# Optimization experiments

Measured on AMD Instinct MI355X. Metric: run time of the kernel, lower is better.

Reference implementation:

```python
import jax, jax.numpy as jnp
import numpy as np

T, N, E = 4, 20000, 640000
D_IN, D_OUT = 256, 128
RRELU_SLOPE = (1.0 / 8.0 + 1.0 / 3.0) / 2.0  # RReLU eval-mode slope


def setup_inputs() -> dict:
    key = jax.random.key(0)
    ks = jax.random.split(key, 16)

    def glorot(k, shape):
        lim = np.sqrt(6.0 / (shape[0] + shape[1]))
        return jax.random.uniform(k, shape, jnp.float32, -lim, lim)

    node_embs = jax.random.normal(ks[0], (T, N, D_IN), jnp.float32)
    edge_index = jax.random.randint(ks[1], (T, 2, E), 0, N, jnp.int32)
    edge_weight = jax.random.uniform(ks[2], (T, E), jnp.float32)
    mask = jnp.zeros((T, N), jnp.float32)
    return {
        "node_embs": node_embs,
        "edge_index": edge_index,
        "edge_weight": edge_weight,
        "mask": mask,
        "p": glorot(ks[3], (D_IN, 1)),
        "Wz": glorot(ks[4], (D_IN, D_IN)),
        "Uz": glorot(ks[5], (D_IN, D_IN)),
        "bz": jnp.zeros((D_IN, D_OUT), jnp.float32),
        "Wr": glorot(ks[6], (D_IN, D_IN)),
        "Ur": glorot(ks[7], (D_IN, D_IN)),
        "br": jnp.zeros((D_IN, D_OUT), jnp.float32),
        "Wh": glorot(ks[8], (D_IN, D_IN)),
        "Uh": glorot(ks[9], (D_IN, D_IN)),
        "bh": jnp.zeros((D_IN, D_OUT), jnp.float32),
        "W0": glorot(ks[10], (D_IN, D_OUT)),
    }


def reference(node_embs, edge_index, edge_weight, mask, p, Wz, Uz, bz, Wr, Ur, br, Wh, Uh, bh, W0):
    n = node_embs.shape[1]
    k = W0.shape[1]

    def step(W, inputs):
        x, ei, w, m = inputs  # x: [N, D_IN]
        # --- TopK summary (EvolveGCN-H) ---
        scores = (x @ p)[:, 0] / jnp.linalg.norm(p) + m  # [N]
        vals, idx = jax.lax.top_k(scores, k)
        xt = (x[idx] * jnp.tanh(vals)[:, None]).T  # [D_IN, k]
        # --- matrix GRU cell: hidden state is the GCN weight W ---
        z = jax.nn.sigmoid(Wz @ xt + Uz @ W + bz)
        r = jax.nn.sigmoid(Wr @ xt + Ur @ W + br)
        h = jnp.tanh(Wh @ xt + Uh @ (r * W) + bh)
        Wn = (1.0 - z) * W + z * h  # [D_IN, D_OUT]
        # --- sparse GCN conv: adj @ (x @ Wn) ---
        y = x @ Wn  # [N, D_OUT]
        dst, src = ei[0], ei[1]
        agg = jax.ops.segment_sum(w[:, None] * y[src], dst, num_segments=n)
        out = jnp.where(agg >= 0, agg, RRELU_SLOPE * agg)
        return Wn, out

    _, out_seq = jax.lax.scan(step, W0, (node_embs, edge_index, edge_weight, mask))
    return out_seq  # [T, N, D_OUT]
```

## Files before the change

kernel.cpp:

```cpp
#include <hip/hip_runtime.h>

typedef unsigned short u16;
typedef unsigned int u32;
typedef unsigned long long u64;

#define T_ 4
#define N_ 20000
#define E_ 640000
#define DIN 256
#define DOUT 128
#define NT (T_*N_)
#define TE (T_*E_)
#define SLOPE 0.22916666666666666f

#define NB 125
#define BNODES 160
#define CAP 5632
#define NBTOT (T_*NB)

#define SGRAN 11
#define NSB 10
#define NBIN (32*NSB*5)
#define NBIN_PAD 2048
#define BOSTRIDE 40

typedef __attribute__((ext_vector_type(8))) short short8;
typedef __attribute__((ext_vector_type(4))) float f32x4;

__device__ __forceinline__ float blo(u32 u) { return __uint_as_float(u << 16); }
__device__ __forceinline__ float bhi(u32 u) { return __uint_as_float(u & 0xFFFF0000u); }
__device__ __forceinline__ u16 f2bf(float f) {
    u32 u = __float_as_uint(f);
    return (u16)((u + 0x7FFFu + ((u >> 16) & 1u)) >> 16);
}
__device__ __forceinline__ u32 fkey(float f) {
    u32 u = __float_as_uint(f);
    return (u & 0x80000000u) ? ~u : (u | 0x80000000u);
}
__device__ __forceinline__ float fkeyinv(u32 k) {
    u32 u = (k & 0x80000000u) ? (k ^ 0x80000000u) : ~k;
    return __uint_as_float(u);
}

__global__ void k_transpose(const float* Wz, const float* Uz, const float* Wr, const float* Ur,
                            const float* Wh, const float* Uh, u32* Tp) {
    int bid = blockIdx.x;
    int m = bid >> 7, b = bid & 127;
    int idx = b * 256 + threadIdx.x;
    int d2 = idx & 127, i = idx >> 7;
    const float* src;
    switch (m) {
        case 0: src = Wz; break;
        case 1: src = Uz; break;
        case 2: src = Wr; break;
        case 3: src = Ur; break;
        case 4: src = Wh; break;
        default: src = Uh; break;
    }
    float lo = src[i * 256 + 2 * d2];
    float hi = src[i * 256 + 2 * d2 + 1];
    Tp[m * 32768 + d2 * 256 + i] = (u32)f2bf(lo) | ((u32)f2bf(hi) << 16);
}

__global__ __launch_bounds__(256) void k_scores(const float* x, const float* p, const float* mask,
                                                float* scores, u16* xb16) {
    __shared__ float pl[256];
    __shared__ float s_invn;
    int tid = threadIdx.x;
    pl[tid] = p[tid];
    __syncthreads();
    if (tid < 64) {
        float v = pl[tid] * pl[tid] + pl[tid + 64] * pl[tid + 64] +
                  pl[tid + 128] * pl[tid + 128] + pl[tid + 192] * pl[tid + 192];
        for (int o = 32; o > 0; o >>= 1) v += __shfl_xor(v, o);
        if (tid == 0) s_invn = 1.0f / sqrtf(v);
    }
    __syncthreads();
    int wid = tid >> 6, lane = tid & 63;
    for (int it = 0; it < 4; ++it) {
        int node = blockIdx.x * 16 + wid * 4 + it;
        const float* row = x + (size_t)node * DIN + lane * 4;
        float4 u = *(const float4*)row;
        float d = u.x * pl[lane * 4 + 0] + u.y * pl[lane * 4 + 1] +
                  u.z * pl[lane * 4 + 2] + u.w * pl[lane * 4 + 3];
        u32 p0 = (u32)f2bf(u.x) | ((u32)f2bf(u.y) << 16);
        u32 p1 = (u32)f2bf(u.z) | ((u32)f2bf(u.w) << 16);
        *(uint2*)(xb16 + (size_t)node * DIN + lane * 4) = make_uint2(p0, p1);
        for (int o = 32; o > 0; o >>= 1) d += __shfl_xor(d, o);
        if (lane == 0) scores[node] = d * s_invn + mask[node];
    }
}

__global__ __launch_bounds__(256) void k_bin(const int* ei, const float* ew,
                                             int* gcur, uint2* binned) {
    int blk = blockIdx.x;
    int t = blk / 250, ci = blk - t * 250;
    int ebase = ci * 2560;
    int tid = threadIdx.x;
    __shared__ u32 hist[128], sc[128], gbase[128];
    __shared__ uint2 stage[2560];
    if (tid < 128) hist[tid] = 0;
    __syncthreads();
    u32 px[10]; u32 pw[10]; u16 rk[10];
#pragma unroll
    for (int k = 0; k < 10; ++k) {
        int e = ebase + tid + k * 256;
        int dst = ei[t * (2 * E_) + e];
        int src = ei[t * (2 * E_) + E_ + e];
        float w = ew[t * E_ + e];
        int b = dst / BNODES;
        int dl = dst - b * BNODES;
        px[k] = (u32)(t * N_ + src) | ((u32)dl << 17) | ((u32)b << 25);
        pw[k] = __float_as_uint(w);
        rk[k] = (u16)atomicAdd(&hist[b], 1u);
    }
    __syncthreads();
    if (tid < 128) sc[tid] = hist[tid];
    __syncthreads();
    for (int o = 1; o < 128; o <<= 1) {
        u32 v = 0;
        if (tid < 128) { v = sc[tid]; if (tid >= o) v += sc[tid - o]; }
        __syncthreads();
        if (tid < 128) sc[tid] = v;
        __syncthreads();
    }
    if (tid < NB) gbase[tid] = (u32)atomicAdd(&gcur[t * NB + tid], (int)hist[tid]);
#pragma unroll
    for (int k = 0; k < 10; ++k) {
        int b = px[k] >> 25;
        u32 slot = (sc[b] - hist[b]) + rk[k];
        stage[slot] = make_uint2(px[k], pw[k]);
    }
    __syncthreads();
    for (int s = tid; s < 2560; s += 256) {
        uint2 v = stage[s];
        int b = v.x >> 25;
        u32 local = gbase[b] + ((u32)s - (sc[b] - hist[b]));
        if (local < CAP)
            binned[(size_t)(t * NB + b) * CAP + local] = v;
    }
}

__global__ __launch_bounds__(512) void k_scatter(const int* gcur, uint2* binned, int* bandoff) {
    int bg = blockIdx.x;
    int t = bg / NB;
    uint2* bucket = binned + (size_t)bg * CAP;
    int cnt = gcur[bg]; if (cnt > CAP) cnt = CAP;
    int tid = threadIdx.x;
    int tbase = t * N_;
    __shared__ u32 nhist[NBIN_PAD];
    __shared__ u32 binstart[NBIN_PAD];
    __shared__ u32 wsum[8];
    for (int i = tid; i < NBIN_PAD; i += 512) nhist[i] = 0;
    __syncthreads();
    u32 vx[11]; u32 vw[11]; u16 r_[11]; u16 bn_[11];
#pragma unroll
    for (int k = 0; k < 11; ++k) {
        int e = tid + k * 512;
        uint2 v;
        if (e < cnt) {
            v = bucket[e];
        } else {
            v = make_uint2(((u32)(e % BNODES) << 17) | (u32)(tbase + N_ - 1), 0u);
        }
        vx[k] = v.x; vw[k] = v.y;
        int dl = (v.x >> 17) & 255;
        int s = (int)(v.x & 0x1FFFFu) - tbase;
        int bin = (dl / 5) * (NSB * 5) + (s >> SGRAN) * 5 + (dl % 5);
        bn_[k] = (u16)bin;
        r_[k] = (u16)atomicAdd(&nhist[bin], 1u);
    }
    __syncthreads();
    u32 loc1, loc2, loc3, tsum;
    {
        int b0 = tid * 4;
        u32 a = nhist[b0], b = nhist[b0 + 1], c = nhist[b0 + 2], d = nhist[b0 + 3];
        loc1 = a; loc2 = a + b; loc3 = a + b + c; tsum = a + b + c + d;
    }
    int lane = tid & 63, wv = tid >> 6;
    u32 xsc = tsum;
    for (int o = 1; o < 64; o <<= 1) { u32 yv = __shfl_up(xsc, o); if (lane >= o) xsc += yv; }
    if (lane == 63) wsum[wv] = xsc;
    __syncthreads();
    u32 wpre = 0;
    for (int wq = 0; wq < wv; ++wq) wpre += wsum[wq];
    u32 tpre = wpre + xsc - tsum;
    {
        int b0 = tid * 4;
        binstart[b0] = tpre;
        binstart[b0 + 1] = tpre + loc1;
        binstart[b0 + 2] = tpre + loc2;
        binstart[b0 + 3] = tpre + loc3;
    }
    __syncthreads();
    if (tid < 33) {
        int v = (tid < 32) ? (int)binstart[tid * (NSB * 5)] : CAP;
        bandoff[bg * BOSTRIDE + tid] = v;
    }
#pragma unroll
    for (int k = 0; k < 11; ++k) {
        u32 pos = binstart[bn_[k]] + r_[k];
        bucket[pos] = make_uint2(vx[k] & 0x1FFFFFFu, vw[k]);
    }
}

__global__ __launch_bounds__(1024) void k_topk(const float* scores, const float* x, float* xtT) {
    int t = blockIdx.x;
    int tid = threadIdx.x;
    const float* sc = scores + t * N_;
    __shared__ u32 hist[256];
    __shared__ u32 sh_dig, sh_need;
    __shared__ u64 sel[256];
    __shared__ u32 selCount;
    __shared__ u32 idxl[128];
    __shared__ float tvl[128];

    u32 kreg[20];
#pragma unroll
    for (int p = 0; p < 20; ++p) {
        int i = tid + p * 1024;
        kreg[p] = (i < N_) ? fkey(sc[i]) : 0u;
    }

    u32 pref = 0;
    u32 need = 128;
    for (int pass = 0; pass < 4; ++pass) {
        int shift = 24 - 8 * pass;
        if (tid < 256) hist[tid] = 0;
        __syncthreads();
#pragma unroll
        for (int p = 0; p < 20; ++p) {
            int i = tid + p * 1024;
            u32 k = kreg[p];
            bool ok = (i < N_) && ((pass == 0) || ((k >> (shift + 8)) == pref));
            if (ok) atomicAdd(&hist[(k >> shift) & 255u], 1u);
        }
        __syncthreads();
        if (tid < 64) {
            int l = tid;
            u32 s = hist[4 * l] + hist[4 * l + 1] + hist[4 * l + 2] + hist[4 * l + 3];
            u32 S = s;
            for (int o = 1; o < 64; o <<= 1) {
                u32 y = __shfl_down(S, o);
                if (l + o < 64) S += y;
            }
            u64 m = __ballot(S >= need);
            int L = 63 - __builtin_clzll(m);
            if (l == L) {
                u32 Snext = S - s;
                u32 r = 0;
                for (int dd = 3; dd >= 0; --dd) {
                    u32 hb = hist[4 * L + dd];
                    r += hb;
                    if (Snext + r >= need) {
                        sh_dig = (u32)(4 * L + dd);
                        sh_need = need - (Snext + r - hb);
                        break;
                    }
                }
            }
        }
        __syncthreads();
        pref = (pref << 8) | sh_dig;
        need = sh_need;
        __syncthreads();
    }
    if (tid == 0) selCount = 0;
    __syncthreads();
    u32 theta = pref;
#pragma unroll
    for (int p = 0; p < 20; ++p) {
        int i = tid + p * 1024;
        u32 k = kreg[p];
        if (i < N_ && k >= theta) {
            u32 pos = atomicAdd(&selCount, 1u);
            if (pos < 256) sel[pos] = (((u64)(k ^ 0xFFFFFFFFu)) << 32) | (u32)i;
        }
    }
    __syncthreads();
    u32 c = selCount;
    if (c > 256) c = 256;
    if (tid < 256 && (u32)tid >= c) sel[tid] = 0xFFFFFFFFFFFFFFFFull;
    __syncthreads();
    for (int k2 = 2; k2 <= 256; k2 <<= 1) {
        for (int jj = k2 >> 1; jj > 0; jj >>= 1) {
            if (tid < 256) {
                int i = tid, ixj = i ^ jj;
                if (ixj > i) {
                    u64 A = sel[i], B = sel[ixj];
                    bool asc = ((i & k2) == 0);
                    bool sw = asc ? (A > B) : (A < B);
                    if (sw) { sel[i] = B; sel[ixj] = A; }
                }
            }
            __syncthreads();
        }
    }
    if (tid < 128) {
        u64 v = sel[tid];
        u32 k = ((u32)(v >> 32)) ^ 0xFFFFFFFFu;
        idxl[tid] = (u32)(v & 0xFFFFFFFFu);
        tvl[tid] = tanhf(fkeyinv(k));
    }
    __syncthreads();
    float* xt_t = xtT + t * (DIN * DOUT);
    const float* xb = x + (size_t)t * N_ * DIN;
    for (int e2 = tid; e2 < DIN * DOUT; e2 += 1024) {
        int j = e2 >> 8, d = e2 & 255;
        xt_t[e2] = xb[(size_t)idxl[j] * DIN + d] * tvl[j];
    }
}

__global__ __launch_bounds__(512) void k_gru(const float* xtT, const float* W0, const u32* Tp,
                                             const float* bz, const float* br, const float* bh,
                                             u16* WnT) {
    int j = blockIdx.x;
    int tid = threadIdx.x;
    int i = tid & 255;
    int h = tid >> 8;
    __shared__ float sxt[256], sW[256], srw[256];
    __shared__ float p1[2][256], p2[2][256];
    const u32* WzT = Tp;
    const u32* UzT = Tp + 32768;
    const u32* WrT = Tp + 65536;
    const u32* UrT = Tp + 98304;
    const u32* WhT = Tp + 131072;
    const u32* UhT = Tp + 163840;
    float wv = W0[i * 128 + j];
    float azb = bz[i * 128 + j];
    float arb = br[i * 128 + j];
    float ahb = bh[i * 128 + j];
    int d2base = h * 64;
    for (int t = 0; t < T_; ++t) {
        __syncthreads();
        if (h == 0) {
            sxt[i] = xtT[t * 32768 + j * 256 + i];
            sW[i] = wv;
        }
        __syncthreads();
        float az = 0.f, ar = 0.f;
#pragma unroll 4
        for (int dd = 0; dd < 64; ++dd) {
            int d2 = d2base + dd;
            float x0 = sxt[2 * d2], x1 = sxt[2 * d2 + 1];
            float w0 = sW[2 * d2], w1 = sW[2 * d2 + 1];
            u32 a = WzT[d2 * 256 + i], b = UzT[d2 * 256 + i];
            u32 cc = WrT[d2 * 256 + i], dv = UrT[d2 * 256 + i];
            az += blo(a) * x0 + bhi(a) * x1 + blo(b) * w0 + bhi(b) * w1;
            ar += blo(cc) * x0 + bhi(cc) * x1 + blo(dv) * w0 + bhi(dv) * w1;
        }
        p1[h][i] = az;
        p2[h][i] = ar;
        __syncthreads();
        float azs = p1[0][i] + p1[1][i] + azb;
        float ars = p2[0][i] + p2[1][i] + arb;
        float z = 1.0f / (1.0f + expf(-azs));
        float r = 1.0f / (1.0f + expf(-ars));
        if (h == 0) srw[i] = r * wv;
        __syncthreads();
        float ah = 0.f;
#pragma unroll 4
        for (int dd = 0; dd < 64; ++dd) {
            int d2 = d2base + dd;
            float x0 = sxt[2 * d2], x1 = sxt[2 * d2 + 1];
            float r0 = srw[2 * d2], r1 = srw[2 * d2 + 1];
            u32 a = WhT[d2 * 256 + i], b = UhT[d2 * 256 + i];
            ah += blo(a) * x0 + bhi(a) * x1 + blo(b) * r0 + bhi(b) * r1;
        }
        p1[h][i] = ah;
        __syncthreads();
        float ahs = p1[0][i] + p1[1][i] + ahb;
        float hh = tanhf(ahs);
        float wn = (1.0f - z) * wv + z * hh;
        if (h == 0) WnT[t * 32768 + j * 256 + i] = f2bf(wn);
        wv = wn;
    }
}

__global__ __launch_bounds__(128) void k_gemm(const u16* xb16, const u16* WnT, u16* y) {
    int t = blockIdx.y;
    const u16* xb = xb16 + (size_t)t * N_ * DIN;
    const u16* Bt = WnT + t * (DIN * DOUT);
    u16* yb = y + (size_t)t * N_ * DOUT;
    int wid = threadIdx.x >> 6, lane = threadIdx.x & 63;
    int quad = lane >> 4, lm = lane & 15;
    int rowBase = blockIdx.x * 64 + wid * 32;
    f32x4 acc[2][8];
#pragma unroll
    for (int mi = 0; mi < 2; ++mi)
#pragma unroll
        for (int ni = 0; ni < 8; ++ni) acc[mi][ni] = (f32x4){0.f, 0.f, 0.f, 0.f};
    size_t aoff[2];
#pragma unroll
    for (int mi = 0; mi < 2; ++mi) {
        int r = rowBase + mi * 16 + lm;
        if (r > N_ - 1) r = N_ - 1;
        aoff[mi] = (size_t)r * DIN + quad * 8;
    }
    const u16* bbase = Bt + lm * 256 + quad * 8;
    for (int kk = 0; kk < 256; kk += 32) {
        short8 a0 = *(const short8*)(xb + aoff[0] + kk);
        short8 a1 = *(const short8*)(xb + aoff[1] + kk);
#pragma unroll
        for (int ni = 0; ni < 8; ++ni) {
            short8 b = *(const short8*)(bbase + ni * 4096 + kk);
            acc[0][ni] = __builtin_amdgcn_mfma_f32_16x16x32_bf16(a0, b, acc[0][ni], 0, 0, 0);
            acc[1][ni] = __builtin_amdgcn_mfma_f32_16x16x32_bf16(a1, b, acc[1][ni], 0, 0, 0);
        }
    }
#pragma unroll
    for (int mi = 0; mi < 2; ++mi)
#pragma unroll
        for (int ni = 0; ni < 8; ++ni)
#pragma unroll
            for (int r = 0; r < 4; ++r) {
                int row = rowBase + mi * 16 + quad * 4 + r;
                if (row < N_) yb[(size_t)row * DOUT + ni * 16 + lm] = f2bf(acc[mi][ni][r]);
            }
}

__global__ __launch_bounds__(512, 4) void k_agg(const uint2* binned, const int* bandoff,
                                                const u16* y, float* out) {
    int bid = blockIdx.x;
    int xcd = bid & 7;
    int t = xcd >> 1;
    int bl = ((bid >> 3) << 1) + (xcd & 1);
    if (bl >= NB) return;
    int bg = t * NB + bl;
    const uint2* bucket = binned + (size_t)bg * CAP;
    const int* bo = bandoff + bg * BOSTRIDE;
    int w = threadIdx.x >> 6, lane = threadIdx.x & 63;
    int q = lane >> 4, lq = lane & 15;
    int Q = (w << 2) | q;
    __shared__ float acc[BNODES][DOUT];
#pragma unroll
    for (int r = 0; r < 20; ++r)
        *(float2*)&acc[w * 20 + r][2 * lane] = make_float2(0.f, 0.f);
    const u16* yq = y + lq * 8;
    int e = bo[Q];
    int eend = bo[Q + 1];
    int curdl = -1;
    float a0 = 0.f, a1 = 0.f, a2 = 0.f, a3 = 0.f, a4 = 0.f, a5 = 0.f, a6 = 0.f, a7 = 0.f;

#define PROC(mm, vv)                                                    \
    {                                                                   \
        int dl = (int)((mm.x >> 17) & 255u);                            \
        if (dl != curdl) {                                              \
            if (curdl >= 0) {                                           \
                float4* rp = (float4*)&acc[curdl][lq * 8];              \
                float4 r0 = rp[0], r1 = rp[1];                          \
                r0.x += a0; r0.y += a1; r0.z += a2; r0.w += a3;         \
                r1.x += a4; r1.y += a5; r1.z += a6; r1.w += a7;         \
                rp[0] = r0; rp[1] = r1;                                 \
            }                                                           \
            a0 = a1 = a2 = a3 = a4 = a5 = a6 = a7 = 0.f;                \
            curdl = dl;                                                 \
        }                                                               \
        float wt = __uint_as_float(mm.y);                               \
        a0 += wt * blo(vv.x); a1 += wt * bhi(vv.x);                     \
        a2 += wt * blo(vv.y); a3 += wt * bhi(vv.y);                     \
        a4 += wt * blo(vv.z); a5 += wt * bhi(vv.z);                     \
        a6 += wt * blo(vv.w); a7 += wt * bhi(vv.w);                     \
    }

    for (; e + 4 <= eend; e += 4) {
        uint2 m0 = bucket[e];
        uint2 m1 = bucket[e + 1];
        uint2 m2 = bucket[e + 2];
        uint2 m3 = bucket[e + 3];
        uint4 v0 = *(const uint4*)(yq + (size_t)(m0.x & 0x1FFFFu) * DOUT);
        uint4 v1 = *(const uint4*)(yq + (size_t)(m1.x & 0x1FFFFu) * DOUT);
        uint4 v2 = *(const uint4*)(yq + (size_t)(m2.x & 0x1FFFFu) * DOUT);
        uint4 v3 = *(const uint4*)(yq + (size_t)(m3.x & 0x1FFFFu) * DOUT);
        PROC(m0, v0)
        PROC(m1, v1)
        PROC(m2, v2)
        PROC(m3, v3)
    }
    for (; e < eend; ++e) {
        uint2 m = bucket[e];
        uint4 v = *(const uint4*)(yq + (size_t)(m.x & 0x1FFFFu) * DOUT);
        PROC(m, v)
    }
    if (curdl >= 0) {
        float4* rp = (float4*)&acc[curdl][lq * 8];
        float4 r0 = rp[0], r1 = rp[1];
        r0.x += a0; r0.y += a1; r0.z += a2; r0.w += a3;
        r1.x += a4; r1.y += a5; r1.z += a6; r1.w += a7;
        rp[0] = r0; rp[1] = r1;
    }
#undef PROC
    int gbase = t * N_ + bl * BNODES + w * 20;
#pragma unroll
    for (int r = 0; r < 20; ++r) {
        float v0 = acc[w * 20 + r][2 * lane], v1 = acc[w * 20 + r][2 * lane + 1];
        v0 = (v0 >= 0.f) ? v0 : SLOPE * v0;
        v1 = (v1 >= 0.f) ? v1 : SLOPE * v1;
        *(float2*)(out + (size_t)(gbase + r) * DOUT + 2 * lane) = make_float2(v0, v1);
    }
}

extern "C" void kernel_launch(void* const* d_in, const int* in_sizes, int n_in,
                              void* d_out, int out_size, void* d_ws, size_t ws_size,
                              hipStream_t stream) {
    const float* x = (const float*)d_in[0];
    const int* ei = (const int*)d_in[1];
    const float* ew = (const float*)d_in[2];
    const float* mask = (const float*)d_in[3];
    const float* p = (const float*)d_in[4];
    const float* Wz = (const float*)d_in[5];
    const float* Uz = (const float*)d_in[6];
    const float* bz = (const float*)d_in[7];
    const float* Wr = (const float*)d_in[8];
    const float* Ur = (const float*)d_in[9];
    const float* br = (const float*)d_in[10];
    const float* Wh = (const float*)d_in[11];
    const float* Uh = (const float*)d_in[12];
    const float* bh = (const float*)d_in[13];
    const float* W0 = (const float*)d_in[14];
    float* out = (float*)d_out;

    char* w = (char*)d_ws;
    u16* xb16 = (u16*)w;        w += (size_t)NT * DIN * 2;
    float* scores = (float*)w;  w += 320256;
    float* xtT = (float*)w;     w += 4 * 32768 * 4;
    u16* WnT = (u16*)w;         w += 4 * 32768 * 2;
    u32* Tp = (u32*)w;          w += 6 * 32768 * 4;
    u16* y = (u16*)w;           w += (size_t)NT * DOUT * 2;
    uint2* binned = (uint2*)w;  w += (size_t)NBTOT * CAP * 8;
    int* gcur = (int*)w;        w += 2048;
    int* bandoff = (int*)w;     w += NBTOT * BOSTRIDE * 4;

    hipMemsetAsync(gcur, 0, 2048, stream);

    k_transpose<<<768, 256, 0, stream>>>(Wz, Uz, Wr, Ur, Wh, Uh, Tp);
    k_scores<<<5000, 256, 0, stream>>>(x, p, mask, scores, xb16);
    k_bin<<<1000, 256, 0, stream>>>(ei, ew, gcur, binned);
    k_scatter<<<NBTOT, 512, 0, stream>>>(gcur, binned, bandoff);
    k_topk<<<4, 1024, 0, stream>>>(scores, x, xtT);
    k_gru<<<128, 512, 0, stream>>>(xtT, W0, Tp, bz, br, bh, WnT);
    k_gemm<<<dim3(313, 4), 128, 0, stream>>>(xb16, WnT, y);
    k_agg<<<512, 512, 0, stream>>>(binned, bandoff, y, out);
}
```

Before: 406.5 us.

## Fuse weight transpose into scores kernel, widen GRU blocks, unroll agg gather by 8

Folds the bf16 weight-transpose work into extra blocks of the scores kernel, removing one kernel launch. It also doubles the GRU kernel's block size to 1024 threads, splitting the reduction over four quarter-slices to shorten each thread's serial loop. Finally it adds an 8-way unrolled gather loop in the aggregation kernel so more row loads are in flight at once. The cost is more registers in agg and more shared-memory reduction traffic in the GRU.

```diff
diff --git a/kernel.cpp b/kernel.cpp
--- a/kernel.cpp
+++ b/kernel.cpp
@@ -42,31 +42,33 @@
     return __uint_as_float(u);
 }
 
-__global__ void k_transpose(const float* Wz, const float* Uz, const float* Wr, const float* Ur,
-                            const float* Wh, const float* Uh, u32* Tp) {
-    int bid = blockIdx.x;
-    int m = bid >> 7, b = bid & 127;
-    int idx = b * 256 + threadIdx.x;
-    int d2 = idx & 127, i = idx >> 7;
-    const float* src;
-    switch (m) {
-        case 0: src = Wz; break;
-        case 1: src = Uz; break;
-        case 2: src = Wr; break;
-        case 3: src = Ur; break;
-        case 4: src = Wh; break;
-        default: src = Uh; break;
-    }
-    float lo = src[i * 256 + 2 * d2];
-    float hi = src[i * 256 + 2 * d2 + 1];
-    Tp[m * 32768 + d2 * 256 + i] = (u32)f2bf(lo) | ((u32)f2bf(hi) << 16);
-}
-
 __global__ __launch_bounds__(256) void k_scores(const float* x, const float* p, const float* mask,
-                                                float* scores, u16* xb16) {
+                                                float* scores, u16* xb16,
+                                                const float* Wz, const float* Uz, const float* Wr,
+                                                const float* Ur, const float* Wh, const float* Uh,
+                                                u32* Tp) {
+    int tid = threadIdx.x;
+    if (blockIdx.x >= 5000) {
+        int bid = blockIdx.x - 5000;
+        int m = bid >> 7, b = bid & 127;
+        int idx = b * 256 + tid;
+        int d2 = idx & 127, i = idx >> 7;
+        const float* src;
+        switch (m) {
+            case 0: src = Wz; break;
+            case 1: src = Uz; break;
+            case 2: src = Wr; break;
+            case 3: src = Ur; break;
+            case 4: src = Wh; break;
+            default: src = Uh; break;
+        }
+        float lo = src[i * 256 + 2 * d2];
+        float hi = src[i * 256 + 2 * d2 + 1];
+        Tp[m * 32768 + d2 * 256 + i] = (u32)f2bf(lo) | ((u32)f2bf(hi) << 16);
+        return;
+    }
     __shared__ float pl[256];
     __shared__ float s_invn;
-    int tid = threadIdx.x;
     pl[tid] = p[tid];
     __syncthreads();
     if (tid < 64) {
@@ -311,15 +313,15 @@
     }
 }
 
-__global__ __launch_bounds__(512) void k_gru(const float* xtT, const float* W0, const u32* Tp,
-                                             const float* bz, const float* br, const float* bh,
-                                             u16* WnT) {
+__global__ __launch_bounds__(1024) void k_gru(const float* xtT, const float* W0, const u32* Tp,
+                                              const float* bz, const float* br, const float* bh,
+                                              u16* WnT) {
     int j = blockIdx.x;
     int tid = threadIdx.x;
     int i = tid & 255;
-    int h = tid >> 8;
+    int qk = tid >> 8;
     __shared__ float sxt[256], sW[256], srw[256];
-    __shared__ float p1[2][256], p2[2][256];
+    __shared__ float p1[4][256], p2[4][256];
     const u32* WzT = Tp;
     const u32* UzT = Tp + 32768;
     const u32* WrT = Tp + 65536;
@@ -330,17 +332,17 @@
     float azb = bz[i * 128 + j];
     float arb = br[i * 128 + j];
     float ahb = bh[i * 128 + j];
-    int d2base = h * 64;
+    int d2base = qk * 32;
     for (int t = 0; t < T_; ++t) {
         __syncthreads();
-        if (h == 0) {
+        if (qk == 0) {
             sxt[i] = xtT[t * 32768 + j * 256 + i];
             sW[i] = wv;
         }
         __syncthreads();
         float az = 0.f, ar = 0.f;
 #pragma unroll 4
-        for (int dd = 0; dd < 64; ++dd) {
+        for (int dd = 0; dd < 32; ++dd) {
             int d2 = d2base + dd;
             float x0 = sxt[2 * d2], x1 = sxt[2 * d2 + 1];
             float w0 = sW[2 * d2], w1 = sW[2 * d2 + 1];
@@ -349,30 +351,30 @@
             az += blo(a) * x0 + bhi(a) * x1 + blo(b) * w0 + bhi(b) * w1;
             ar += blo(cc) * x0 + bhi(cc) * x1 + blo(dv) * w0 + bhi(dv) * w1;
         }
-        p1[h][i] = az;
-        p2[h][i] = ar;
-        __syncthreads();
-        float azs = p1[0][i] + p1[1][i] + azb;
-        float ars = p2[0][i] + p2[1][i] + arb;
+        p1[qk][i] = az;
+        p2[qk][i] = ar;
+        __syncthreads();
+        float azs = p1[0][i] + p1[1][i] + p1[2][i] + p1[3][i] + azb;
+        float ars = p2[0][i] + p2[1][i] + p2[2][i] + p2[3][i] + arb;
         float z = 1.0f / (1.0f + expf(-azs));
         float r = 1.0f / (1.0f + expf(-ars));
-        if (h == 0) srw[i] = r * wv;
+        if (qk == 0) srw[i] = r * wv;
         __syncthreads();
         float ah = 0.f;
 #pragma unroll 4
-        for (int dd = 0; dd < 64; ++dd) {
+        for (int dd = 0; dd < 32; ++dd) {
             int d2 = d2base + dd;
             float x0 = sxt[2 * d2], x1 = sxt[2 * d2 + 1];
             float r0 = srw[2 * d2], r1 = srw[2 * d2 + 1];
             u32 a = WhT[d2 * 256 + i], b = UhT[d2 * 256 + i];
             ah += blo(a) * x0 + bhi(a) * x1 + blo(b) * r0 + bhi(b) * r1;
         }
-        p1[h][i] = ah;
-        __syncthreads();
-        float ahs = p1[0][i] + p1[1][i] + ahb;
+        p1[qk][i] = ah;
+        __syncthreads();
+        float ahs = p1[0][i] + p1[1][i] + p1[2][i] + p1[3][i] + ahb;
         float hh = tanhf(ahs);
         float wn = (1.0f - z) * wv + z * hh;
-        if (h == 0) WnT[t * 32768 + j * 256 + i] = f2bf(wn);
+        if (qk == 0) WnT[t * 32768 + j * 256 + i] = f2bf(wn);
         wv = wn;
     }
 }
@@ -463,6 +465,32 @@
         a6 += wt * blo(vv.w); a7 += wt * bhi(vv.w);                     \
     }
 
+    for (; e + 8 <= eend; e += 8) {
+        uint2 m0 = bucket[e];
+        uint2 m1 = bucket[e + 1];
+        uint2 m2 = bucket[e + 2];
+        uint2 m3 = bucket[e + 3];
+        uint2 m4 = bucket[e + 4];
+        uint2 m5 = bucket[e + 5];
+        uint2 m6 = bucket[e + 6];
+        uint2 m7 = bucket[e + 7];
+        uint4 v0 = *(const uint4*)(yq + (size_t)(m0.x & 0x1FFFFu) * DOUT);
+        uint4 v1 = *(const uint4*)(yq + (size_t)(m1.x & 0x1FFFFu) * DOUT);
+        uint4 v2 = *(const uint4*)(yq + (size_t)(m2.x & 0x1FFFFu) * DOUT);
+        uint4 v3 = *(const uint4*)(yq + (size_t)(m3.x & 0x1FFFFu) * DOUT);
+        uint4 v4 = *(const uint4*)(yq + (size_t)(m4.x & 0x1FFFFu) * DOUT);
+        uint4 v5 = *(const uint4*)(yq + (size_t)(m5.x & 0x1FFFFu) * DOUT);
+        uint4 v6 = *(const uint4*)(yq + (size_t)(m6.x & 0x1FFFFu) * DOUT);
+        uint4 v7 = *(const uint4*)(yq + (size_t)(m7.x & 0x1FFFFu) * DOUT);
+        PROC(m0, v0)
+        PROC(m1, v1)
+        PROC(m2, v2)
+        PROC(m3, v3)
+        PROC(m4, v4)
+        PROC(m5, v5)
+        PROC(m6, v6)
+        PROC(m7, v7)
+    }
     for (; e + 4 <= eend; e += 4) {
         uint2 m0 = bucket[e];
         uint2 m1 = bucket[e + 1];
@@ -533,12 +561,11 @@
 
     hipMemsetAsync(gcur, 0, 2048, stream);
 
-    k_transpose<<<768, 256, 0, stream>>>(Wz, Uz, Wr, Ur, Wh, Uh, Tp);
-    k_scores<<<5000, 256, 0, stream>>>(x, p, mask, scores, xb16);
+    k_scores<<<5768, 256, 0, stream>>>(x, p, mask, scores, xb16, Wz, Uz, Wr, Ur, Wh, Uh, Tp);
     k_bin<<<1000, 256, 0, stream>>>(ei, ew, gcur, binned);
     k_scatter<<<NBTOT, 512, 0, stream>>>(gcur, binned, bandoff);
     k_topk<<<4, 1024, 0, stream>>>(scores, x, xtT);
-    k_gru<<<128, 512, 0, stream>>>(xtT, W0, Tp, bz, br, bh, WnT);
+    k_gru<<<128, 1024, 0, stream>>>(xtT, W0, Tp, bz, br, bh, WnT);
     k_gemm<<<dim3(313, 4), 128, 0, stream>>>(xb16, WnT, y);
     k_agg<<<512, 512, 0, stream>>>(binned, bandoff, y, out);
 }
```

Result: faster. 386.5 us (-4.9%).
